# Performance work log

Hardware: AMD Instinct MI355X
Metric: run time of the kernel (lower is better)

The kernel has to match this reference:

```python
import jax, jax.numpy as jnp
import numpy as np

DIM = 256
GRID = 5


def setup_inputs() -> dict:
    key = jax.random.key(0)
    kx, kw = jax.random.split(key)
    x = jax.random.normal(kx, (32, 2048, DIM), dtype=jnp.float32)
    scale = 1.0 / (np.sqrt(DIM) * np.sqrt(GRID))
    fourier_weight = jax.random.normal(kw, (2, DIM, DIM, GRID), dtype=jnp.float32) * scale
    bias = jnp.zeros((DIM,), dtype=jnp.float32)
    return {"x": x, "fourier_weight": fourier_weight, "bias": bias}


def reference(x, fourier_weight, bias):
    D = bias.shape[0]
    G = fourier_weight.shape[-1]
    out_shape = x.shape[:-1] + (D,)
    xf = x.reshape(-1, D)                                  # (N, D)
    k = jnp.arange(1, G + 1, dtype=x.dtype)                # (G,)
    arg = xf[:, :, None] * k                               # (N, D, G)
    # y[n,o] = sum_{d,g} cos(k_g x[n,d]) W[0,o,d,g] + sin(k_g x[n,d]) W[1,o,d,g] + b[o]
    y = jnp.einsum('ndg,odg->no', jnp.cos(arg), fourier_weight[0])
    y = y + jnp.einsum('ndg,odg->no', jnp.sin(arg), fourier_weight[1])
    y = y + bias
    return y.reshape(out_shape)
```

## Files before the change

kernel.cpp:

```cpp
#include <hip/hip_runtime.h>
#include <hip/hip_bf16.h>
#include <stdint.h>

#define DIM 256
#define GRID_G 5
#define KTOT 2560
#define BM 128
#define BN 256
#define BK 64
#define NTHREADS 256
#define NCHUNK (KTOT / BK)
#define AS_SH (BM * BK)

typedef float f32x4 __attribute__((ext_vector_type(4)));
typedef short bf16x8 __attribute__((ext_vector_type(8)));

static __device__ __forceinline__ uint32_t f2bf_bits(float v) {
    uint32_t u = __float_as_uint(v);
    return (u + 0x7FFFu + ((u >> 16) & 1u)) >> 16;
}

__global__ void wtransform(const float* __restrict__ W, uint16_t* __restrict__ Wb) {
    int t = blockIdx.x * blockDim.x + threadIdx.x;
    if (t >= DIM * KTOT / 8) return;
    int o  = t / (KTOT / 8);
    int k8 = t - o * (KTOT / 8);
    int k0 = k8 * 8;
    int g  = k0 >> 9;
    int r  = k0 & 511;
    int d0 = r >> 1;
    union { uint16_t v[8]; uint4 q; } u;
#pragma unroll
    for (int j = 0; j < 8; ++j) {
        int d = d0 + (j >> 1);
        int s = j & 1;
        float w = W[(((s * DIM + o) * DIM + d) * GRID_G) + g];
        u.v[j] = (uint16_t)f2bf_bits(w);
    }
    *(uint4*)((char*)Wb + (size_t)t * 16) = u.q;
}

__global__ __launch_bounds__(NTHREADS, 2)
void fourier_gemm(const float* __restrict__ x, const uint16_t* __restrict__ Wb,
                  const float* __restrict__ bias, float* __restrict__ out) {
    __shared__ __align__(16) short As[2 * AS_SH];

    const int tid  = threadIdx.x;
    const int lane = tid & 63;
    const int wcol = tid >> 6;
    const int row0 = blockIdx.x * BM;
    const int q16  = (lane >> 4) << 4;
    const int l15  = lane & 15;

    f32x4 acc[8][4];
#pragma unroll
    for (int m = 0; m < 8; ++m)
#pragma unroll
        for (int n = 0; n < 4; ++n)
            acc[m][n] = (f32x4){0.f, 0.f, 0.f, 0.f};

    const int sd2 = tid & 15;
    const int sn  = tid >> 4;

    float2 xq[8];

#define LOAD_X(dr_)                                                           \
    {                                                                         \
        _Pragma("unroll")                                                     \
        for (int i = 0; i < 8; ++i) {                                         \
            int n = sn + i * 16;                                              \
            xq[i] = *(const float2*)&x[(size_t)(row0 + n) * DIM +             \
                                       (dr_) * 32 + 2 * sd2];                 \
        }                                                                     \
    }

#define TRIG_WRITE(kg1, buf)                                                  \
    {                                                                         \
        float kgrev = (float)(kg1) * 0.15915494309189535f;                    \
        char* abase = (char*)(As + (buf) * AS_SH);                            \
        _Pragma("unroll")                                                     \
        for (int i = 0; i < 8; ++i) {                                         \
            int n = sn + i * 16;                                              \
            float r0 = xq[i].x * kgrev;                                       \
            float r1 = xq[i].y * kgrev;                                       \
            float s0, c0, s1, c1;                                             \
            asm("v_sin_f32 %0, %1" : "=v"(s0) : "v"(r0));                     \
            asm("v_cos_f32 %0, %1" : "=v"(c0) : "v"(r0));                     \
            asm("v_sin_f32 %0, %1" : "=v"(s1) : "v"(r1));                     \
            asm("v_cos_f32 %0, %1" : "=v"(c1) : "v"(r1));                     \
            uint32_t p0, p1;                                                  \
            asm("v_cvt_pk_bf16_f32 %0, %1, %2" : "=v"(p0) : "v"(c0), "v"(s0));\
            asm("v_cvt_pk_bf16_f32 %0, %1, %2" : "=v"(p1) : "v"(c1), "v"(s1));\
            int boff = (n * 128 + sd2 * 8) ^ ((n & 7) << 4);                  \
            uint64_t pk = ((uint64_t)p1 << 32) | (uint64_t)p0;                \
            *(uint64_t*)(abase + boff) = pk;                                  \
        }                                                                     \
    }

    LOAD_X(0);
    TRIG_WRITE(1, 0);
    __syncthreads();

    int it = 0;
    for (int dr = 0; dr < 8; ++dr) {
#pragma unroll
        for (int g = 0; g < GRID_G; ++g, ++it) {
            const int cur = it & 1;
            const int c   = g * 8 + dr;
            const char* Ac = (const char*)(As + cur * AS_SH);

            if (g == GRID_G - 1 && dr < 7) { LOAD_X(dr + 1); }

#pragma unroll
            for (int ks = 0; ks < 2; ++ks) {
                bf16x8 bfr[4], af[8];
#pragma unroll
                for (int nf = 0; nf < 4; ++nf) {
                    int o = wcol * 64 + nf * 16 + l15;
                    bfr[nf] = *(const bf16x8*)((const char*)Wb +
                              (size_t)o * (KTOT * 2) + c * 128 + ks * 64 + q16);
                }
#pragma unroll
                for (int m = 0; m < 8; ++m) {
                    int rr  = m * 16 + l15;
                    int off = (rr * 128 + ks * 64 + q16) ^ ((rr & 7) << 4);
                    af[m] = *(const bf16x8*)(Ac + off);
                }
#pragma unroll
                for (int m = 0; m < 8; ++m)
#pragma unroll
                    for (int nf = 0; nf < 4; ++nf)
                        acc[m][nf] = __builtin_amdgcn_mfma_f32_16x16x32_bf16(
                            af[m], bfr[nf], acc[m][nf], 0, 0, 0);
            }

            if (it < NCHUNK - 1) {
                int kgn = (g == GRID_G - 1) ? 1 : (g + 2);
                TRIG_WRITE(kgn, cur ^ 1);
            }
            __syncthreads();
        }
    }

#pragma unroll
    for (int nf = 0; nf < 4; ++nf) {
        int ocol = wcol * 64 + nf * 16 + l15;
        float b = bias[ocol];
#pragma unroll
        for (int m = 0; m < 8; ++m) {
            int rbase = row0 + m * 16 + ((lane >> 4) << 2);
#pragma unroll
            for (int r2 = 0; r2 < 4; ++r2) {
                out[(size_t)(rbase + r2) * DIM + ocol] = acc[m][nf][r2] + b;
            }
        }
    }
}

extern "C" void kernel_launch(void* const* d_in, const int* in_sizes, int n_in,
                              void* d_out, int out_size, void* d_ws, size_t ws_size,
                              hipStream_t stream) {
    const float* x    = (const float*)d_in[0];
    const float* W    = (const float*)d_in[1];
    const float* bias = (const float*)d_in[2];
    float* out        = (float*)d_out;
    uint16_t* Wb      = (uint16_t*)d_ws;

    int rows = in_sizes[0] / DIM;
    int wthreads = DIM * KTOT / 8;

    hipLaunchKernelGGL(wtransform, dim3((wthreads + 255) / 256), dim3(256), 0, stream, W, Wb);
    hipLaunchKernelGGL(fourier_gemm, dim3(rows / BM), dim3(NTHREADS), 0, stream,
                       x, Wb, bias, out);
}
```

Baseline: 234.6 us.

## Double tile height to 256 rows with 8 waves and software-pipelined W prefetch

Each block now covers 256 rows with 512 threads (2x4 wave grid), so each W tile loaded is reused across twice as many rows. The loop over chunks is fully unrolled, with register double-buffering of W fragments and x loads, so the next chunk's global loads are issued before the current MFMAs. The trig LDS writes are placed between the two MFMA k-steps, with setprio raised around the MFMAs and explicit barriers. In exchange, occupancy drops to one block per CU, the grid halves to 256 blocks, and register pressure rises.

```diff
diff --git a/kernel.cpp b/kernel.cpp
--- a/kernel.cpp
+++ b/kernel.cpp
@@ -5,12 +5,11 @@
 #define DIM 256
 #define GRID_G 5
 #define KTOT 2560
-#define BM 128
+#define BM 256
 #define BN 256
 #define BK 64
-#define NTHREADS 256
-#define NCHUNK (KTOT / BK)
-#define AS_SH (BM * BK)
+#define NTHREADS 512
+#define AS_BYTES (BM * BK * 2)
 
 typedef float f32x4 __attribute__((ext_vector_type(4)));
 typedef short bf16x8 __attribute__((ext_vector_type(8)));
@@ -40,17 +39,21 @@
     *(uint4*)((char*)Wb + (size_t)t * 16) = u.q;
 }
 
-__global__ __launch_bounds__(NTHREADS, 2)
+__global__ __launch_bounds__(NTHREADS, 1)
 void fourier_gemm(const float* __restrict__ x, const uint16_t* __restrict__ Wb,
                   const float* __restrict__ bias, float* __restrict__ out) {
-    __shared__ __align__(16) short As[2 * AS_SH];
+    __shared__ __align__(16) char As[2 * AS_BYTES];
 
     const int tid  = threadIdx.x;
     const int lane = tid & 63;
-    const int wcol = tid >> 6;
+    const int wave = tid >> 6;
+    const int wrow = wave >> 2;
+    const int wcol = wave & 3;
     const int row0 = blockIdx.x * BM;
     const int q16  = (lane >> 4) << 4;
     const int l15  = lane & 15;
+    const int sd2  = tid & 15;
+    const int sn   = tid >> 4;
 
     f32x4 acc[8][4];
 #pragma unroll
@@ -59,30 +62,40 @@
         for (int n = 0; n < 4; ++n)
             acc[m][n] = (f32x4){0.f, 0.f, 0.f, 0.f};
 
-    const int sd2 = tid & 15;
-    const int sn  = tid >> 4;
-
-    float2 xq[8];
-
-#define LOAD_X(dr_)                                                           \
-    {                                                                         \
+    float2 xqA[8], xqB[8];
+    bf16x8 bfA[8], bfB[8];
+
+#define ISSUE_B(c_, B_)                                                       \
+    {                                                                         \
+        _Pragma("unroll")                                                     \
+        for (int ks = 0; ks < 2; ++ks)                                        \
+        _Pragma("unroll")                                                     \
+        for (int nf = 0; nf < 4; ++nf) {                                      \
+            int o = wcol * 64 + nf * 16 + l15;                                \
+            B_[ks * 4 + nf] = *(const bf16x8*)((const char*)Wb +              \
+                (size_t)o * (KTOT * 2) + (c_) * 128 + ks * 64 + q16);         \
+        }                                                                     \
+    }
+
+#define LOAD_X(dr_, XQ_)                                                     \
+    {                                                                        \
+        _Pragma("unroll")                                                    \
+        for (int i = 0; i < 8; ++i) {                                        \
+            int n = sn + i * 32;                                             \
+            XQ_[i] = *(const float2*)&x[(size_t)(row0 + n) * DIM +           \
+                                        (dr_) * 32 + 2 * sd2];               \
+        }                                                                    \
+    }
+
+#define TRIG_WRITE(kg1, XQ_, abase_)                                          \
+    {                                                                         \
+        float kgrev = (float)(kg1) * 0.15915494309189535f;                    \
+        char* abase = (abase_);                                               \
         _Pragma("unroll")                                                     \
         for (int i = 0; i < 8; ++i) {                                         \
-            int n = sn + i * 16;                                              \
-            xq[i] = *(const float2*)&x[(size_t)(row0 + n) * DIM +             \
-                                       (dr_) * 32 + 2 * sd2];                 \
-        }                                                                     \
-    }
-
-#define TRIG_WRITE(kg1, buf)                                                  \
-    {                                                                         \
-        float kgrev = (float)(kg1) * 0.15915494309189535f;                    \
-        char* abase = (char*)(As + (buf) * AS_SH);                            \
-        _Pragma("unroll")                                                     \
-        for (int i = 0; i < 8; ++i) {                                         \
-            int n = sn + i * 16;                                              \
-            float r0 = xq[i].x * kgrev;                                       \
-            float r1 = xq[i].y * kgrev;                                       \
+            int n = sn + i * 32;                                              \
+            float r0 = XQ_[i].x * kgrev;                                      \
+            float r1 = XQ_[i].y * kgrev;                                      \
             float s0, c0, s1, c1;                                             \
             asm("v_sin_f32 %0, %1" : "=v"(s0) : "v"(r0));                     \
             asm("v_cos_f32 %0, %1" : "=v"(c0) : "v"(r0));                     \
@@ -97,49 +110,63 @@
         }                                                                     \
     }
 
-    LOAD_X(0);
-    TRIG_WRITE(1, 0);
-    __syncthreads();
-
-    int it = 0;
-    for (int dr = 0; dr < 8; ++dr) {
-#pragma unroll
-        for (int g = 0; g < GRID_G; ++g, ++it) {
-            const int cur = it & 1;
-            const int c   = g * 8 + dr;
-            const char* Ac = (const char*)(As + cur * AS_SH);
-
-            if (g == GRID_G - 1 && dr < 7) { LOAD_X(dr + 1); }
-
-#pragma unroll
-            for (int ks = 0; ks < 2; ++ks) {
-                bf16x8 bfr[4], af[8];
-#pragma unroll
-                for (int nf = 0; nf < 4; ++nf) {
-                    int o = wcol * 64 + nf * 16 + l15;
-                    bfr[nf] = *(const bf16x8*)((const char*)Wb +
-                              (size_t)o * (KTOT * 2) + c * 128 + ks * 64 + q16);
-                }
-#pragma unroll
-                for (int m = 0; m < 8; ++m) {
-                    int rr  = m * 16 + l15;
-                    int off = (rr * 128 + ks * 64 + q16) ^ ((rr & 7) << 4);
-                    af[m] = *(const bf16x8*)(Ac + off);
-                }
-#pragma unroll
-                for (int m = 0; m < 8; ++m)
-#pragma unroll
-                    for (int nf = 0; nf < 4; ++nf)
-                        acc[m][nf] = __builtin_amdgcn_mfma_f32_16x16x32_bf16(
-                            af[m], bfr[nf], acc[m][nf], 0, 0, 0);
-            }
-
-            if (it < NCHUNK - 1) {
-                int kgn = (g == GRID_G - 1) ? 1 : (g + 2);
-                TRIG_WRITE(kgn, cur ^ 1);
-            }
-            __syncthreads();
-        }
+#define MFMA_KS(ks_, Ac_, B_)                                                 \
+    {                                                                         \
+        bf16x8 af[8];                                                         \
+        _Pragma("unroll")                                                     \
+        for (int m = 0; m < 8; ++m) {                                         \
+            int rr  = wrow * 128 + m * 16 + l15;                              \
+            int off = (rr * 128 + (ks_) * 64 + q16) ^ ((rr & 7) << 4);        \
+            af[m] = *(const bf16x8*)((Ac_) + off);                            \
+        }                                                                     \
+        __builtin_amdgcn_s_setprio(1);                                        \
+        _Pragma("unroll")                                                     \
+        for (int m = 0; m < 8; ++m)                                           \
+        _Pragma("unroll")                                                     \
+        for (int nf = 0; nf < 4; ++nf)                                        \
+            acc[m][nf] = __builtin_amdgcn_mfma_f32_16x16x32_bf16(             \
+                af[m], B_[(ks_) * 4 + nf], acc[m][nf], 0, 0, 0);              \
+        __builtin_amdgcn_s_setprio(0);                                        \
+    }
+
+#define CHUNK(ccur_, cnxt_, BCUR_, BNXT_, ACUR_, ANXT_, kgn_, XQ_, doiss_, dotrig_) \
+    {                                                                         \
+        if (doiss_) { ISSUE_B(cnxt_, BNXT_); }                                \
+        MFMA_KS(0, ACUR_, BCUR_);                                             \
+        if (dotrig_) { TRIG_WRITE(kgn_, XQ_, ANXT_); }                        \
+        MFMA_KS(1, ACUR_, BCUR_);                                             \
+        asm volatile("s_waitcnt lgkmcnt(0)" ::: "memory");                    \
+        __builtin_amdgcn_s_barrier();                                         \
+        __builtin_amdgcn_sched_barrier(0);                                    \
+    }
+
+    char* buf0 = (char*)As;
+    char* buf1 = (char*)As + AS_BYTES;
+
+    ISSUE_B(0, bfA);
+    LOAD_X(0, xqA);
+    TRIG_WRITE(1, xqA, buf0);
+    asm volatile("s_waitcnt lgkmcnt(0)" ::: "memory");
+    __builtin_amdgcn_s_barrier();
+    __builtin_amdgcn_sched_barrier(0);
+
+    for (int dr2 = 0; dr2 < 4; ++dr2) {
+        const int drA = 2 * dr2;
+        const int drB = 2 * dr2 + 1;
+        const bool more = (dr2 < 3);
+
+         CHUNK(drA,       8 + drA,  bfA, bfB, buf0, buf1, 2, xqA, true, true);
+         CHUNK(8 + drA,  16 + drA,  bfB, bfA, buf1, buf0, 3, xqA, true, true);
+         CHUNK(16 + drA, 24 + drA,  bfA, bfB, buf0, buf1, 4, xqA, true, true);
+         LOAD_X(drB, xqB);
+                     CHUNK(24 + drA, 32 + drA,  bfB, bfA, buf1, buf0, 5, xqA, true, true);
+         CHUNK(32 + drA, drB,       bfA, bfB, buf0, buf1, 1, xqB, true, true);
+         CHUNK(drB,       8 + drB,  bfB, bfA, buf1, buf0, 2, xqB, true, true);
+         CHUNK(8 + drB,  16 + drB,  bfA, bfB, buf0, buf1, 3, xqB, true, true);
+         CHUNK(16 + drB, 24 + drB,  bfB, bfA, buf1, buf0, 4, xqB, true, true);
+         if (more) { LOAD_X(drA + 2, xqA); }
+                     CHUNK(24 + drB, 32 + drB,  bfA, bfB, buf0, buf1, 5, xqB, true, true);
+         CHUNK(32 + drB, drB + 1,   bfB, bfA, buf1, buf0, 1, xqA, more, more);
     }
 
 #pragma unroll
@@ -148,13 +175,19 @@
         float b = bias[ocol];
 #pragma unroll
         for (int m = 0; m < 8; ++m) {
-            int rbase = row0 + m * 16 + ((lane >> 4) << 2);
+            int rbase = row0 + wrow * 128 + m * 16 + ((lane >> 4) << 2);
 #pragma unroll
             for (int r2 = 0; r2 < 4; ++r2) {
                 out[(size_t)(rbase + r2) * DIM + ocol] = acc[m][nf][r2] + b;
             }
         }
     }
+
+#undef ISSUE_B
+#undef LOAD_X
+#undef TRIG_WRITE
+#undef MFMA_KS
+#undef CHUNK
 }
 
 extern "C" void kernel_launch(void* const* d_in, const int* in_sizes, int n_in,
```

New measurement: 427.2 us. 82.1% more time.
